# Optimization experiments

Measured on AMD Instinct MI355X. Metric: run time of the kernel, lower is better.

## Reference

```python
import jax, jax.numpy as jnp
import numpy as np

N, E = 100000, 1600000
IN_DIM, H, D = 128, 4, 32
ALPHA = 0.2  # leaky relu negative slope


def setup_inputs() -> dict:
    key = jax.random.key(0)
    k1, k2, k3, k4, k5, k6 = jax.random.split(key, 6)
    return {
        "inputs": jax.random.normal(k1, (N, IN_DIM), dtype=jnp.float32),
        "src": jax.random.randint(k2, (E,), 0, N, dtype=jnp.int32),
        "dst": jax.random.randint(k3, (E,), 0, N, dtype=jnp.int32),
        "fc_w": jax.random.normal(k4, (IN_DIM, H * D), dtype=jnp.float32) * (1.414 / np.sqrt(IN_DIM)),
        "attn_l": jax.random.normal(k5, (D,), dtype=jnp.float32) * 0.1,
        "attn_r": jax.random.normal(k6, (D,), dtype=jnp.float32) * 0.1,
    }


def reference(inputs, src, dst, fc_w, attn_l, attn_r):
    # fc + reshape to (N, H, D); feat_drop is identity (p=0)
    ft = (inputs @ fc_w).reshape(N, H, D)
    # attn_l/attn_r are (1,1,D) in torch -> broadcast over heads
    a1 = jnp.einsum("nhd,d->nh", ft, attn_l)  # (N, H)
    a2 = jnp.einsum("nhd,d->nh", ft, attn_r)  # (N, H)
    # per-edge logits; original keeps ONLY head-0 scores after edge_softmax
    # (scores[:, 0, :].unsqueeze(1)), so we only need head 0 here.
    e = jax.nn.leaky_relu(a1[src, 0] + a2[dst, 0], ALPHA)  # (E,)
    # numerically-stable segment softmax over destination nodes
    emax = jax.ops.segment_max(e, dst, num_segments=N)
    ex = jnp.exp(e - emax[dst])
    denom = jax.ops.segment_sum(ex, dst, num_segments=N)
    a = ex / denom[dst]  # (E,) broadcast to all heads
    # u_mul_e + sum aggregation; attn_drop is identity (p=0)
    msg = ft[src] * a[:, None, None]  # (E, H, D)
    out = jax.ops.segment_sum(msg, dst, num_segments=N)  # (N, H, D)
    return out
```

## Files before the change

kernel.cpp:

```cpp
#include <hip/hip_runtime.h>


#define ALPHA 0.2f
#define NBLK 512
#define BBITS 8
#define BSIZE 256
#define CAP 5120

typedef __attribute__((ext_vector_type(8))) short bf16x8;
typedef __attribute__((ext_vector_type(8))) unsigned short u16x8;
typedef __attribute__((ext_vector_type(4))) float f32x4;

__device__ __forceinline__ unsigned short f2bf(float f) {
    unsigned u = __float_as_uint(f);
    unsigned r = (u + 0x7FFFu + ((u >> 16) & 1u)) >> 16;
    return (unsigned short)r;
}
__device__ __forceinline__ float bf2f(unsigned short h) {
    return __uint_as_float(((unsigned)h) << 16);
}

__global__ __launch_bounds__(256) void prep_kernel(const float* __restrict__ W,
                                                   u16x8* __restrict__ Wswz) {
    int gt = blockIdx.x * 256 + threadIdx.x;
    if (gt < 2048) {
        int n = gt >> 4, c = gt & 15;
        u16x8 v;
        #pragma unroll
        for (int j = 0; j < 8; ++j) v[j] = f2bf(W[(c * 8 + j) * 128 + n]);
        Wswz[n * 16 + (c ^ (n & 7))] = v;
    }
}

__global__ __launch_bounds__(256) void gemm_kernel(
        const float* __restrict__ A, const u16x8* __restrict__ Wswz,
        const float* __restrict__ attn_l, const float* __restrict__ attn_r,
        unsigned short* __restrict__ ftb,
        float* __restrict__ s_l, float* __restrict__ s_r, int N) {
    __shared__ u16x8 A_lds[1024];
    __shared__ u16x8 W_lds[2048];
    const int tid = threadIdx.x;
    const int block_row = blockIdx.x * 64;

    for (int i = tid; i < 2048; i += 256) W_lds[i] = Wswz[i];

    for (int l = tid; l < 1024; l += 256) {
        int m = l >> 4, c = l & 15;
        int row = block_row + m;
        float4 v0 = make_float4(0.f, 0.f, 0.f, 0.f), v1 = v0;
        if (row < N) {
            const float4* p = (const float4*)(A + (size_t)row * 128 + c * 8);
            v0 = p[0]; v1 = p[1];
        }
        u16x8 u;
        u[0] = f2bf(v0.x); u[1] = f2bf(v0.y); u[2] = f2bf(v0.z); u[3] = f2bf(v0.w);
        u[4] = f2bf(v1.x); u[5] = f2bf(v1.y); u[6] = f2bf(v1.z); u[7] = f2bf(v1.w);
        A_lds[m * 16 + (c ^ (m & 7))] = u;
    }
    __syncthreads();

    const int wv = tid >> 6;
    const int lane = tid & 63;
    const int lm = lane & 15;
    const int quad = lane >> 4;

    f32x4 acc[8];
    #pragma unroll
    for (int t = 0; t < 8; ++t) acc[t] = (f32x4)(0.f);

    const int am = wv * 16 + lm;
    #pragma unroll
    for (int ks = 0; ks < 4; ++ks) {
        int c = ks * 4 + quad;
        bf16x8 af = *(const bf16x8*)&A_lds[am * 16 + (c ^ (am & 7))];
        #pragma unroll
        for (int t = 0; t < 8; ++t) {
            int n = t * 16 + lm;
            bf16x8 bf = *(const bf16x8*)&W_lds[n * 16 + (c ^ (n & 7))];
            acc[t] = __builtin_amdgcn_mfma_f32_16x16x32_bf16(af, bf, acc[t], 0, 0, 0);
        }
    }

    {
        float al0 = attn_l[lm], al1 = attn_l[16 + lm];
        float ar0 = attn_r[lm], ar1 = attn_r[16 + lm];
        #pragma unroll
        for (int r = 0; r < 4; ++r) {
            float pl = acc[0][r] * al0 + acc[1][r] * al1;
            float pr = acc[0][r] * ar0 + acc[1][r] * ar1;
            #pragma unroll
            for (int mask = 1; mask < 16; mask <<= 1) {
                pl += __shfl_xor(pl, mask, 64);
                pr += __shfl_xor(pr, mask, 64);
            }
            if (lm == 0) {
                int row = block_row + wv * 16 + quad * 4 + r;
                if (row < N) { s_l[row] = pl; s_r[row] = pr; }
            }
        }
    }

    unsigned short* C_lds = (unsigned short*)A_lds;
    #pragma unroll
    for (int t = 0; t < 8; ++t) {
        #pragma unroll
        for (int r = 0; r < 4; ++r) {
            int mrow = wv * 16 + quad * 4 + r;
            C_lds[mrow * 128 + t * 16 + lm] = f2bf(acc[t][r]);
        }
    }
    __syncthreads();
    for (int l = tid; l < 1024; l += 256) {
        int m = l >> 4, c = l & 15;
        int row = block_row + m;
        if (row < N)
            *(u16x8*)(ftb + (size_t)row * 128 + c * 8) = *(const u16x8*)&C_lds[m * 128 + c * 8];
    }
}

__global__ __launch_bounds__(256) void bhist_kernel(const int* __restrict__ dst,
                                                    unsigned* __restrict__ bh,
                                                    int E, int nbucket, int slice) {
    __shared__ unsigned cnt[512];
    for (int i = threadIdx.x; i < nbucket; i += 256) cnt[i] = 0u;
    __syncthreads();
    const int b = blockIdx.x;
    int s0 = b * slice, s1 = min(s0 + slice, E);
    for (int i = s0 + threadIdx.x; i < s1; i += 256)
        atomicAdd(&cnt[((unsigned)dst[i]) >> BBITS], 1u);
    __syncthreads();
    for (int k = threadIdx.x; k < nbucket; k += 256)
        bh[(size_t)k * NBLK + b] = cnt[k];
}

__global__ __launch_bounds__(256) void scan1_kernel(const unsigned* __restrict__ counts,
                                                    unsigned* __restrict__ S,
                                                    unsigned* __restrict__ partials, int M) {
    __shared__ unsigned sh[256];
    const int tid = threadIdx.x;
    const int base = blockIdx.x * 1024 + tid * 4;
    unsigned v[4];
    unsigned s = 0;
    #pragma unroll
    for (int k = 0; k < 4; ++k) {
        int idx = base + k;
        v[k] = (idx < M) ? counts[idx] : 0u;
        s += v[k];
    }
    sh[tid] = s;
    __syncthreads();
    for (int off = 1; off < 256; off <<= 1) {
        unsigned t = (tid >= off) ? sh[tid - off] : 0u;
        __syncthreads();
        sh[tid] += t;
        __syncthreads();
    }
    if (tid == 255) partials[blockIdx.x] = sh[255];
    unsigned run = (tid == 0) ? 0u : sh[tid - 1];
    #pragma unroll
    for (int k = 0; k < 4; ++k) {
        int idx = base + k;
        if (idx < M) S[idx] = run;
        run += v[k];
    }
}

__global__ __launch_bounds__(256) void scan2_kernel(unsigned* __restrict__ partials, int NB) {
    __shared__ unsigned sh[256];
    const int tid = threadIdx.x;
    unsigned v[4];
    unsigned s = 0;
    #pragma unroll
    for (int k = 0; k < 4; ++k) {
        int idx = tid * 4 + k;
        v[k] = (idx < NB) ? partials[idx] : 0u;
        s += v[k];
    }
    sh[tid] = s;
    __syncthreads();
    for (int off = 1; off < 256; off <<= 1) {
        unsigned t = (tid >= off) ? sh[tid - off] : 0u;
        __syncthreads();
        sh[tid] += t;
        __syncthreads();
    }
    unsigned run = (tid == 0) ? 0u : sh[tid - 1];
    #pragma unroll
    for (int k = 0; k < 4; ++k) {
        int idx = tid * 4 + k;
        if (idx < NB) partials[idx] = run;
        run += v[k];
    }
}

__global__ void scan3_kernel(unsigned* __restrict__ S,
                             const unsigned* __restrict__ partials, int M) {
    int i = blockIdx.x * 256 + threadIdx.x;
    if (i < M) S[i] += partials[i >> 10];
}

__global__ __launch_bounds__(256) void bscatter_kernel(
        const int* __restrict__ src, const int* __restrict__ dst,
        const float* __restrict__ s_l, const float* __restrict__ s_r,
        const unsigned* __restrict__ S, uint2* __restrict__ staged,
        int E, int nbucket, int slice) {
    __shared__ unsigned cur[512];
    for (int i = threadIdx.x; i < nbucket; i += 256) cur[i] = 0u;
    __syncthreads();
    const int b = blockIdx.x;
    int s0 = b * slice, s1 = min(s0 + slice, E);
    for (int i = s0 + threadIdx.x; i < s1; i += 256) {
        int s = src[i], d = dst[i];
        unsigned k = ((unsigned)d) >> BBITS;
        float x = s_l[s] + s_r[d];
        float e = (x > 0.f) ? x : ALPHA * x;
        unsigned pos = S[(size_t)k * NBLK + b] + atomicAdd(&cur[k], 1u);
        staged[pos] = make_uint2((unsigned)s | (((unsigned)d & (BSIZE - 1)) << 20),
                                 __float_as_uint(e));
    }
}

__global__ __launch_bounds__(256) void bsort_kernel(
        uint2* __restrict__ staged, const unsigned* __restrict__ S,
        unsigned* __restrict__ offsets, int N, int E, int nbucket) {
    __shared__ uint2 rec[CAP];
    __shared__ unsigned cnt[BSIZE], incl[BSIZE], cur[BSIZE];
    const int k = blockIdx.x;
    const int t = threadIdx.x;
    unsigned gstart = S[(size_t)k * NBLK];
    unsigned gend = (k + 1 == nbucket) ? (unsigned)E : S[(size_t)(k + 1) * NBLK];
    int n = (int)(gend - gstart);
    if (n > CAP) n = CAP;

    cnt[t] = 0u;
    __syncthreads();
    for (int i = t; i < n; i += 256)
        atomicAdd(&cnt[staged[gstart + i].x >> 20], 1u);
    __syncthreads();
    incl[t] = cnt[t];
    __syncthreads();
    for (int off = 1; off < 256; off <<= 1) {
        unsigned u = (t >= off) ? incl[t - off] : 0u;
        __syncthreads();
        incl[t] += u;
        __syncthreads();
    }
    cur[t] = 0u;
    __syncthreads();
    for (int i = t; i < n; i += 256) {
        uint2 r = staged[gstart + i];
        unsigned dl = r.x >> 20;
        unsigned p = incl[dl] - cnt[dl] + atomicAdd(&cur[dl], 1u);
        rec[p] = r;
    }
    __syncthreads();
    int d = k * BSIZE + t;
    if (d < N) {
        int b0 = (int)(incl[t] - cnt[t]);
        int c = (int)cnt[t];
        float m = -1e30f;
        for (int j = 0; j < c; ++j) m = fmaxf(m, __uint_as_float(rec[b0 + j].y));
        float sum = 0.f;
        for (int j = 0; j < c; ++j) sum += __expf(__uint_as_float(rec[b0 + j].y) - m);
        float rden = (c > 0) ? 1.f / sum : 0.f;
        for (int j = 0; j < c; ++j) {
            float a = __expf(__uint_as_float(rec[b0 + j].y) - m) * rden;
            rec[b0 + j].y = __float_as_uint(a);
        }
        offsets[d] = gstart + incl[t];
    }
    __syncthreads();
    for (int i = t; i < n; i += 256) {
        uint2 r = rec[i];
        staged[gstart + i] = make_uint2(r.x & 0xFFFFFu, r.y);
    }
}

__global__ __launch_bounds__(256) void aggregate_kernel(
        const uint2* __restrict__ edata, const unsigned* __restrict__ offsets,
        const unsigned short* __restrict__ ftb, float* __restrict__ out, int N) {
    int wv = threadIdx.x >> 6;
    int lane = threadIdx.x & 63;
    int d = blockIdx.x * 4 + wv;
    if (d >= N) return;

    unsigned start = (d == 0) ? 0u : offsets[d - 1];
    unsigned end = offsets[d];

    int eh = lane >> 5, j = lane & 31;
    float4 acc = make_float4(0.f, 0.f, 0.f, 0.f);
    unsigned e = start + eh;
    for (; e + 2 < end; e += 4) {
        uint2 ed0 = edata[e];
        uint2 ed1 = edata[e + 2];
        ushort4 q0 = *(const ushort4*)(ftb + (size_t)ed0.x * 128 + j * 4);
        ushort4 q1 = *(const ushort4*)(ftb + (size_t)ed1.x * 128 + j * 4);
        float a0 = __uint_as_float(ed0.y);
        float a1 = __uint_as_float(ed1.y);
        acc.x += a0 * bf2f(q0.x) + a1 * bf2f(q1.x);
        acc.y += a0 * bf2f(q0.y) + a1 * bf2f(q1.y);
        acc.z += a0 * bf2f(q0.z) + a1 * bf2f(q1.z);
        acc.w += a0 * bf2f(q0.w) + a1 * bf2f(q1.w);
    }
    for (; e < end; e += 2) {
        uint2 ed = edata[e];
        ushort4 q = *(const ushort4*)(ftb + (size_t)ed.x * 128 + j * 4);
        float a = __uint_as_float(ed.y);
        acc.x += a * bf2f(q.x);
        acc.y += a * bf2f(q.y);
        acc.z += a * bf2f(q.z);
        acc.w += a * bf2f(q.w);
    }

    acc.x += __shfl_xor(acc.x, 32, 64);
    acc.y += __shfl_xor(acc.y, 32, 64);
    acc.z += __shfl_xor(acc.z, 32, 64);
    acc.w += __shfl_xor(acc.w, 32, 64);
    if (eh == 0)
        ((float4*)out)[(size_t)d * 32 + j] = acc;
}

static inline size_t align256(size_t x) { return (x + 255) & ~(size_t)255; }

extern "C" void kernel_launch(void* const* d_in, const int* in_sizes, int n_in,
                              void* d_out, int out_size, void* d_ws, size_t ws_size,
                              hipStream_t stream) {
    const float* inputs = (const float*)d_in[0];
    const int*   src    = (const int*)d_in[1];
    const int*   dst    = (const int*)d_in[2];
    const float* fc_w   = (const float*)d_in[3];
    const float* attn_l = (const float*)d_in[4];
    const float* attn_r = (const float*)d_in[5];
    float* out = (float*)d_out;

    const int N = in_sizes[0] / 128;
    const int E = in_sizes[1];
    const int nbucket = (N + BSIZE - 1) / BSIZE;
    const int M = nbucket * NBLK;
    const int NB1 = (M + 1023) / 1024;
    const int slice = (E + NBLK - 1) / NBLK;

    char* w = (char*)d_ws;
    unsigned short* ftb = (unsigned short*)w;  w += align256((size_t)N * 128 * 2);
    float*    s_l      = (float*)w;     w += align256((size_t)N * 4);
    float*    s_r      = (float*)w;     w += align256((size_t)N * 4);
    unsigned* bh       = (unsigned*)w;  w += align256((size_t)M * 4);
    unsigned* S        = (unsigned*)w;  w += align256((size_t)M * 4);
    unsigned* partials = (unsigned*)w;  w += align256(1024 * 4);
    unsigned* offsets  = (unsigned*)w;  w += align256((size_t)N * 4);
    u16x8*    Wswz     = (u16x8*)w;     w += align256(2048 * 16);
    uint2*    staged   = (uint2*)w;     w += align256((size_t)E * 8);

    prep_kernel<<<8, 256, 0, stream>>>(fc_w, Wswz);
    gemm_kernel<<<(N + 63) / 64, 256, 0, stream>>>(inputs, Wswz, attn_l, attn_r,
                                                   ftb, s_l, s_r, N);
    bhist_kernel<<<NBLK, 256, 0, stream>>>(dst, bh, E, nbucket, slice);
    scan1_kernel<<<NB1, 256, 0, stream>>>(bh, S, partials, M);
    scan2_kernel<<<1, 256, 0, stream>>>(partials, NB1);
    scan3_kernel<<<(M + 255) / 256, 256, 0, stream>>>(S, partials, M);
    bscatter_kernel<<<NBLK, 256, 0, stream>>>(src, dst, s_l, s_r, S, staged,
                                              E, nbucket, slice);
    bsort_kernel<<<nbucket, 256, 0, stream>>>(staged, S, offsets, N, E, nbucket);
    aggregate_kernel<<<(N + 3) / 4, 256, 0, stream>>>(staged, offsets, ftb, out, N);
}
```

Before: 276.2 us.

## Fuse histogram into GEMM launch, fold scan3 into consumers, widen aggregate loads

The bucket histogram now runs as extra blocks of the GEMM kernel, so the two independent stages share one launch. The scan3 pass is dropped: bscatter and bsort add the block partials themselves, and bscatter caches its per-bucket bases in shared memory. The aggregate kernel now handles four edges per step and reads 16-byte feature chunks per lane, unpacking bf16 with shifts and masks. Together these cut launch count and global round trips and improve gather width. The cost is more shuffles per output and bucket-count reads that are no longer reused.

Measured after the change: 255.8 us. 1.08x faster.

```diff
diff --git a/kernel.cpp b/kernel.cpp
--- a/kernel.cpp
+++ b/kernel.cpp
@@ -15,9 +15,6 @@
     unsigned u = __float_as_uint(f);
     unsigned r = (u + 0x7FFFu + ((u >> 16) & 1u)) >> 16;
     return (unsigned short)r;
-}
-__device__ __forceinline__ float bf2f(unsigned short h) {
-    return __uint_as_float(((unsigned)h) << 16);
 }
 
 __global__ __launch_bounds__(256) void prep_kernel(const float* __restrict__ W,
@@ -32,14 +29,32 @@
     }
 }
 
-__global__ __launch_bounds__(256) void gemm_kernel(
+__global__ __launch_bounds__(256) void front_kernel(
         const float* __restrict__ A, const u16x8* __restrict__ Wswz,
         const float* __restrict__ attn_l, const float* __restrict__ attn_r,
         unsigned short* __restrict__ ftb,
-        float* __restrict__ s_l, float* __restrict__ s_r, int N) {
-    __shared__ u16x8 A_lds[1024];
-    __shared__ u16x8 W_lds[2048];
+        float* __restrict__ s_l, float* __restrict__ s_r, int N, int GB,
+        const int* __restrict__ dst, unsigned* __restrict__ bh,
+        int E, int nbucket, int slice) {
+    __shared__ char smem[49152];
     const int tid = threadIdx.x;
+
+    if (blockIdx.x >= (unsigned)GB) {
+        unsigned* cnt = (unsigned*)smem;
+        for (int i = tid; i < nbucket; i += 256) cnt[i] = 0u;
+        __syncthreads();
+        const int b = blockIdx.x - GB;
+        int s0 = b * slice, s1 = min(s0 + slice, E);
+        for (int i = s0 + tid; i < s1; i += 256)
+            atomicAdd(&cnt[((unsigned)dst[i]) >> BBITS], 1u);
+        __syncthreads();
+        for (int k = tid; k < nbucket; k += 256)
+            bh[(size_t)k * NBLK + b] = cnt[k];
+        return;
+    }
+
+    u16x8* A_lds = (u16x8*)smem;
+    u16x8* W_lds = (u16x8*)(smem + 16384);
     const int block_row = blockIdx.x * 64;
 
     for (int i = tid; i < 2048; i += 256) W_lds[i] = Wswz[i];
@@ -118,21 +133,6 @@
     }
 }
 
-__global__ __launch_bounds__(256) void bhist_kernel(const int* __restrict__ dst,
-                                                    unsigned* __restrict__ bh,
-                                                    int E, int nbucket, int slice) {
-    __shared__ unsigned cnt[512];
-    for (int i = threadIdx.x; i < nbucket; i += 256) cnt[i] = 0u;
-    __syncthreads();
-    const int b = blockIdx.x;
-    int s0 = b * slice, s1 = min(s0 + slice, E);
-    for (int i = s0 + threadIdx.x; i < s1; i += 256)
-        atomicAdd(&cnt[((unsigned)dst[i]) >> BBITS], 1u);
-    __syncthreads();
-    for (int k = threadIdx.x; k < nbucket; k += 256)
-        bh[(size_t)k * NBLK + b] = cnt[k];
-}
-
 __global__ __launch_bounds__(256) void scan1_kernel(const unsigned* __restrict__ counts,
                                                     unsigned* __restrict__ S,
                                                     unsigned* __restrict__ partials, int M) {
@@ -193,28 +193,27 @@
     }
 }
 
-__global__ void scan3_kernel(unsigned* __restrict__ S,
-                             const unsigned* __restrict__ partials, int M) {
-    int i = blockIdx.x * 256 + threadIdx.x;
-    if (i < M) S[i] += partials[i >> 10];
-}
-
 __global__ __launch_bounds__(256) void bscatter_kernel(
         const int* __restrict__ src, const int* __restrict__ dst,
         const float* __restrict__ s_l, const float* __restrict__ s_r,
-        const unsigned* __restrict__ S, uint2* __restrict__ staged,
-        int E, int nbucket, int slice) {
+        const unsigned* __restrict__ S, const unsigned* __restrict__ partials,
+        uint2* __restrict__ staged, int E, int nbucket, int slice) {
+    __shared__ unsigned basel[512];
     __shared__ unsigned cur[512];
-    for (int i = threadIdx.x; i < nbucket; i += 256) cur[i] = 0u;
-    __syncthreads();
     const int b = blockIdx.x;
+    for (int k = threadIdx.x; k < nbucket; k += 256) {
+        unsigned idx = (unsigned)k * NBLK + b;
+        basel[k] = S[idx] + partials[idx >> 10];
+        cur[k] = 0u;
+    }
+    __syncthreads();
     int s0 = b * slice, s1 = min(s0 + slice, E);
     for (int i = s0 + threadIdx.x; i < s1; i += 256) {
         int s = src[i], d = dst[i];
         unsigned k = ((unsigned)d) >> BBITS;
         float x = s_l[s] + s_r[d];
         float e = (x > 0.f) ? x : ALPHA * x;
-        unsigned pos = S[(size_t)k * NBLK + b] + atomicAdd(&cur[k], 1u);
+        unsigned pos = basel[k] + atomicAdd(&cur[k], 1u);
         staged[pos] = make_uint2((unsigned)s | (((unsigned)d & (BSIZE - 1)) << 20),
                                  __float_as_uint(e));
     }
@@ -222,13 +221,16 @@
 
 __global__ __launch_bounds__(256) void bsort_kernel(
         uint2* __restrict__ staged, const unsigned* __restrict__ S,
+        const unsigned* __restrict__ partials,
         unsigned* __restrict__ offsets, int N, int E, int nbucket) {
     __shared__ uint2 rec[CAP];
     __shared__ unsigned cnt[BSIZE], incl[BSIZE], cur[BSIZE];
     const int k = blockIdx.x;
     const int t = threadIdx.x;
-    unsigned gstart = S[(size_t)k * NBLK];
-    unsigned gend = (k + 1 == nbucket) ? (unsigned)E : S[(size_t)(k + 1) * NBLK];
+    unsigned idx0 = (unsigned)k * NBLK;
+    unsigned gstart = S[idx0] + partials[idx0 >> 10];
+    unsigned gend = (k + 1 == nbucket) ? (unsigned)E
+                                       : (S[idx0 + NBLK] + partials[(idx0 + NBLK) >> 10]);
     int n = (int)(gend - gstart);
     if (n > CAP) n = CAP;
 
@@ -283,41 +285,41 @@
     int lane = threadIdx.x & 63;
     int d = blockIdx.x * 4 + wv;
     if (d >= N) return;
+    int eh = lane >> 4;
+    int j  = lane & 15;
 
     unsigned start = (d == 0) ? 0u : offsets[d - 1];
     unsigned end = offsets[d];
 
-    int eh = lane >> 5, j = lane & 31;
-    float4 acc = make_float4(0.f, 0.f, 0.f, 0.f);
-    unsigned e = start + eh;
-    for (; e + 2 < end; e += 4) {
-        uint2 ed0 = edata[e];
-        uint2 ed1 = edata[e + 2];
-        ushort4 q0 = *(const ushort4*)(ftb + (size_t)ed0.x * 128 + j * 4);
-        ushort4 q1 = *(const ushort4*)(ftb + (size_t)ed1.x * 128 + j * 4);
-        float a0 = __uint_as_float(ed0.y);
-        float a1 = __uint_as_float(ed1.y);
-        acc.x += a0 * bf2f(q0.x) + a1 * bf2f(q1.x);
-        acc.y += a0 * bf2f(q0.y) + a1 * bf2f(q1.y);
-        acc.z += a0 * bf2f(q0.z) + a1 * bf2f(q1.z);
-        acc.w += a0 * bf2f(q0.w) + a1 * bf2f(q1.w);
-    }
-    for (; e < end; e += 2) {
-        uint2 ed = edata[e];
-        ushort4 q = *(const ushort4*)(ftb + (size_t)ed.x * 128 + j * 4);
-        float a = __uint_as_float(ed.y);
-        acc.x += a * bf2f(q.x);
-        acc.y += a * bf2f(q.y);
-        acc.z += a * bf2f(q.z);
-        acc.w += a * bf2f(q.w);
-    }
-
-    acc.x += __shfl_xor(acc.x, 32, 64);
-    acc.y += __shfl_xor(acc.y, 32, 64);
-    acc.z += __shfl_xor(acc.z, 32, 64);
-    acc.w += __shfl_xor(acc.w, 32, 64);
-    if (eh == 0)
-        ((float4*)out)[(size_t)d * 32 + j] = acc;
+    float acc[8] = {0.f, 0.f, 0.f, 0.f, 0.f, 0.f, 0.f, 0.f};
+    for (unsigned e = start; e < end; e += 8) {
+        unsigned i0 = e + eh, i1 = e + 4 + eh;
+        uint2 d0 = (i0 < end) ? edata[i0] : make_uint2(0u, 0u);
+        uint2 d1 = (i1 < end) ? edata[i1] : make_uint2(0u, 0u);
+        uint4 q0 = *(const uint4*)(ftb + (size_t)d0.x * 128 + j * 8);
+        uint4 q1 = *(const uint4*)(ftb + (size_t)d1.x * 128 + j * 8);
+        float a0 = __uint_as_float(d0.y);
+        float a1 = __uint_as_float(d1.y);
+        const unsigned* w0 = (const unsigned*)&q0;
+        const unsigned* w1 = (const unsigned*)&q1;
+        #pragma unroll
+        for (int p = 0; p < 4; ++p) {
+            acc[2 * p]     += a0 * __uint_as_float(w0[p] << 16);
+            acc[2 * p + 1] += a0 * __uint_as_float(w0[p] & 0xFFFF0000u);
+            acc[2 * p]     += a1 * __uint_as_float(w1[p] << 16);
+            acc[2 * p + 1] += a1 * __uint_as_float(w1[p] & 0xFFFF0000u);
+        }
+    }
+    #pragma unroll
+    for (int p = 0; p < 8; ++p) {
+        acc[p] += __shfl_xor(acc[p], 16, 64);
+        acc[p] += __shfl_xor(acc[p], 32, 64);
+    }
+    if (eh == 0) {
+        float4* op = (float4*)(out + (size_t)d * 128 + j * 8);
+        op[0] = make_float4(acc[0], acc[1], acc[2], acc[3]);
+        op[1] = make_float4(acc[4], acc[5], acc[6], acc[7]);
+    }
 }
 
 static inline size_t align256(size_t x) { return (x + 255) & ~(size_t)255; }
@@ -339,6 +341,7 @@
     const int M = nbucket * NBLK;
     const int NB1 = (M + 1023) / 1024;
     const int slice = (E + NBLK - 1) / NBLK;
+    const int GB = (N + 63) / 64;
 
     char* w = (char*)d_ws;
     unsigned short* ftb = (unsigned short*)w;  w += align256((size_t)N * 128 * 2);
@@ -352,14 +355,14 @@
     uint2*    staged   = (uint2*)w;     w += align256((size_t)E * 8);
 
     prep_kernel<<<8, 256, 0, stream>>>(fc_w, Wswz);
-    gemm_kernel<<<(N + 63) / 64, 256, 0, stream>>>(inputs, Wswz, attn_l, attn_r,
-                                                   ftb, s_l, s_r, N);
-    bhist_kernel<<<NBLK, 256, 0, stream>>>(dst, bh, E, nbucket, slice);
+    front_kernel<<<GB + NBLK, 256, 0, stream>>>(inputs, Wswz, attn_l, attn_r,
+                                                ftb, s_l, s_r, N, GB,
+                                                dst, bh, E, nbucket, slice);
     scan1_kernel<<<NB1, 256, 0, stream>>>(bh, S, partials, M);
     scan2_kernel<<<1, 256, 0, stream>>>(partials, NB1);
-    scan3_kernel<<<(M + 255) / 256, 256, 0, stream>>>(S, partials, M);
-    bscatter_kernel<<<NBLK, 256, 0, stream>>>(src, dst, s_l, s_r, S, staged,
-                                              E, nbucket, slice);
-    bsort_kernel<<<nbucket, 256, 0, stream>>>(staged, S, offsets, N, E, nbucket);
+    bscatter_kernel<<<NBLK, 256, 0, stream>>>(src, dst, s_l, s_r, S, partials,
+                                              staged, E, nbucket, slice);
+    bsort_kernel<<<nbucket, 256, 0, stream>>>(staged, S, partials, offsets,
+                                              N, E, nbucket);
     aggregate_kernel<<<(N + 3) / 4, 256, 0, stream>>>(staged, offsets, ftb, out, N);
 }
```
